# Optimization experiments

Hardware: AMD Instinct MI355X
Metric: run time of the kernel (lower is better)

## Reference

```python
import jax, jax.numpy as jnp
import numpy as np

B, S, T = 32, 128, 64
V = 32000   # src_vocab_size == tgt_vocab_size
E = 512     # rnn_input_size
H = 512     # rnn_hidden_size
PAD = 0


def lstm_cell(x, h, c, wih, whh, bih, bhh):
    # PyTorch gate order: i, f, g, o
    gates = x @ wih.T + h @ whh.T + bih + bhh
    i, f, g, o = jnp.split(gates, 4, axis=-1)
    c = jax.nn.sigmoid(f) * c + jax.nn.sigmoid(i) * jnp.tanh(g)
    h = jax.nn.sigmoid(o) * jnp.tanh(c)
    return h, c


def _encode(src, enc_emb, wih_f, whh_f, bih_f, bhh_f, wih_r, whh_r, bih_r, bhh_r):
    xs = enc_emb[src].transpose(1, 0, 2)  # [S, B, E]
    b = src.shape[0]

    def run(wih, whh, bih, bhh, reverse):
        def step(carry, x):
            h, c = carry
            h, c = lstm_cell(x, h, c, wih, whh, bih, bhh)
            return (h, c), None
        init = (jnp.zeros((b, H), xs.dtype), jnp.zeros((b, H), xs.dtype))
        (h, c), _ = jax.lax.scan(step, init, xs, reverse=reverse)
        return h, c

    hf, cf = run(wih_f, whh_f, bih_f, bhh_f, False)
    hr, cr = run(wih_r, whh_r, bih_r, bhh_r, True)
    return jnp.stack([hf, hr]), jnp.stack([cf, cr])  # (2, B, H)


def _forward(src, tgt, enc_emb, dec_emb,
             enc_wih_f, enc_whh_f, enc_bih_f, enc_bhh_f,
             enc_wih_r, enc_whh_r, enc_bih_r, enc_bhh_r,
             dec_wih_f, dec_whh_f, dec_bih_f, dec_bhh_f,
             dec_wih_r, dec_whh_r, dec_bih_r, dec_bhh_r,
             cls_w, cls_b):
    h0, c0 = _encode(src, enc_emb, enc_wih_f, enc_whh_f, enc_bih_f, enc_bhh_f,
                     enc_wih_r, enc_whh_r, enc_bih_r, enc_bhh_r)

    def step(carry, _):
        dec_in, h, c = carry
        x = dec_emb[dec_in]                      # [B, E]
        hf, cf = lstm_cell(x, h[0], c[0], dec_wih_f, dec_whh_f, dec_bih_f, dec_bhh_f)
        hr, cr = lstm_cell(x, h[1], c[1], dec_wih_r, dec_whh_r, dec_bih_r, dec_bhh_r)
        logits = jnp.concatenate([hf, hr], -1) @ cls_w.T + cls_b  # [B, V]
        nxt = jnp.argmax(logits, -1).astype(dec_in.dtype)         # sampling_ratio=0 branch
        return (nxt, jnp.stack([hf, hr]), jnp.stack([cf, cr])), logits

    init = (tgt[:, 0], h0, c0)
    _, outs = jax.lax.scan(step, init, None, length=tgt.shape[1] - 1)
    outs = outs.transpose(1, 0, 2)  # [B, T-1, V]
    zeros = jnp.zeros((tgt.shape[0], 1, outs.shape[-1]), outs.dtype)  # timestep 0 left zero
    return jnp.concatenate([zeros, outs], axis=1)  # [B, T, V]


def setup_inputs():
    key = jax.random.key(0)
    ks = jax.random.split(key, 24)
    sc = 1.0 / np.sqrt(H)

    def w(k, shape):
        return jax.random.uniform(k, shape, jnp.float32, -sc, sc)

    src = jax.random.randint(ks[0], (B, S), 0, V)
    tgt = jax.random.randint(ks[1], (B, T), 0, V)
    enc_emb = (jax.random.normal(ks[2], (V, E), jnp.float32) * 0.02).at[PAD].set(0.0)
    dec_emb = (jax.random.normal(ks[3], (V, E), jnp.float32) * 0.02).at[PAD].set(0.0)
    return {
        "src": src, "tgt": tgt,
        "enc_emb": enc_emb, "dec_emb": dec_emb,
        "enc_wih_f": w(ks[4], (4 * H, E)), "enc_whh_f": w(ks[5], (4 * H, H)),
        "enc_bih_f": w(ks[6], (4 * H,)), "enc_bhh_f": w(ks[7], (4 * H,)),
        "enc_wih_r": w(ks[8], (4 * H, E)), "enc_whh_r": w(ks[9], (4 * H, H)),
        "enc_bih_r": w(ks[10], (4 * H,)), "enc_bhh_r": w(ks[11], (4 * H,)),
        "dec_wih_f": w(ks[12], (4 * H, E)), "dec_whh_f": w(ks[13], (4 * H, H)),
        "dec_bih_f": w(ks[14], (4 * H,)), "dec_bhh_f": w(ks[15], (4 * H,)),
        "dec_wih_r": w(ks[16], (4 * H, E)), "dec_whh_r": w(ks[17], (4 * H, H)),
        "dec_bih_r": w(ks[18], (4 * H,)), "dec_bhh_r": w(ks[19], (4 * H,)),
        "cls_w": w(ks[20], (V, 2 * H)), "cls_b": w(ks[21], (V,)),
    }


def reference(src, tgt, enc_emb, dec_emb,
              enc_wih_f, enc_whh_f, enc_bih_f, enc_bhh_f,
              enc_wih_r, enc_whh_r, enc_bih_r, enc_bhh_r,
              dec_wih_f, dec_whh_f, dec_bih_f, dec_bhh_f,
              dec_wih_r, dec_whh_r, dec_bih_r, dec_bhh_r,
              cls_w, cls_b):
    return _forward(src, tgt, enc_emb, dec_emb,
                    enc_wih_f, enc_whh_f, enc_bih_f, enc_bhh_f,
                    enc_wih_r, enc_whh_r, enc_bih_r, enc_bhh_r,
                    dec_wih_f, dec_whh_f, dec_bih_f, dec_bhh_f,
                    dec_wih_r, dec_whh_r, dec_bih_r, dec_bhh_r,
                    cls_w, cls_b)
```

## Files before the change

kernel.cpp:

```cpp
#include <hip/hip_runtime.h>
#include <stdint.h>


#define NT 1024
#define NBLK 256

constexpr int HSTR = 580;
constexpr int XSTR = 1156;
constexpr unsigned LDS_ENC = 78336;
constexpr unsigned LDS_CELL = 150016;
constexpr unsigned LDS_CLS = 150528;

constexpr size_t OFF_AMAX  = 0;
constexpr size_t OFF_FLAGS = 16128;
constexpr size_t OFF_XG    = 17408;
constexpr size_t OFF_HENC  = OFF_XG + 67108864ULL;
constexpr size_t OFF_HCAT  = OFF_HENC + 262144ULL;
constexpr size_t OFF_CST   = OFF_HCAT + 262144ULL;

__device__ __forceinline__ float sigm(float x) {
  if (x >= 0.f) return 1.f / (1.f + expf(-x));
  float e = expf(x);
  return e / (1.f + e);
}

__device__ __forceinline__ void fma4(const float4& w, const float4& h, float4& a) {
  a.x = fmaf(w.x, h.x, a.x);
  a.y = fmaf(w.y, h.y, a.y);
  a.z = fmaf(w.z, h.z, a.z);
  a.w = fmaf(w.w, h.w, a.w);
}

__device__ __forceinline__ float hsum4(const float4& a) {
  return (a.x + a.y) + (a.z + a.w);
}

__device__ __forceinline__ float dot4(const float4& w, const float4& h, float acc) {
  return fmaf(w.x, h.x, fmaf(w.y, h.y, fmaf(w.z, h.z, fmaf(w.w, h.w, acc))));
}

__device__ __forceinline__ unsigned long long lgkey(float lg, int vr) {
  unsigned u = __float_as_uint(lg);
  u = (u & 0x80000000u) ? ~u : (u | 0x80000000u);
  return ((unsigned long long)u << 32) | (0xFFFFFFFFu - (unsigned)vr);
}

__global__ __launch_bounds__(NT) void k_xg(
    const int* __restrict__ src, const float* __restrict__ enc_emb,
    const float* __restrict__ ewih_f, const float* __restrict__ ebih_f,
    const float* __restrict__ ebhh_f,
    const float* __restrict__ ewih_r, const float* __restrict__ ebih_r,
    const float* __restrict__ ebhh_r,
    float* __restrict__ Xg, float* __restrict__ h_enc, float* __restrict__ out) {
  extern __shared__ float smem[];
  const int tid = threadIdx.x;
  const int bid = blockIdx.x;
  const int d  = bid >> 7;
  const int u0 = (bid & 127) << 2;

  float* hL  = smem;

  const int rgE = tid >> 7;
  const int bpE = (tid >> 4) & 7;
  const int ksE = tid & 15;
  const int r0E = rgE * 2, r1E = r0E + 1;
  const int growE0 = (r0E & 3) * 512 + u0 + (r0E >> 2);
  const int growE1 = (r1E & 3) * 512 + u0 + (r1E >> 2);

  const float* ewih = d ? ewih_r : ewih_f;
  const float* ebih = d ? ebih_r : ebih_f;
  const float* ebhh = d ? ebhh_r : ebhh_f;

  float4 wA[8], wB[8];
#pragma unroll
  for (int i4 = 0; i4 < 8; ++i4) {
    wA[i4] = *(const float4*)(ewih + (size_t)growE0 * 512 + ksE * 32 + i4 * 4);
    wB[i4] = *(const float4*)(ewih + (size_t)growE1 * 512 + ksE * 32 + i4 * 4);
  }
  const float biasA = ebih[growE0] + ebhh[growE0];
  const float biasB = ebih[growE1] + ebhh[growE1];

  for (int t = 0; t < 128; ++t) {
    {
      int b = tid >> 5, i = tid & 31;
      int tok = src[b * 128 + t];
      const float* row = enc_emb + (size_t)tok * 512;
#pragma unroll
      for (int q = 0; q < 4; ++q) {
        int k = (i + 32 * q) * 4;
        float4 v = *(const float4*)(row + k);
        int pc = k + ((k >> 5) << 2);
        *(float4*)(hL + b * HSTR + pc) = v;
      }
    }
    __syncthreads();
    for (int gi = 0; gi < 4; ++gi) {
      int b = bpE * 4 + gi;
      const float* hb = hL + b * HSTR + ksE * 36;
      float4 a0 = {0, 0, 0, 0}, a1 = {0, 0, 0, 0};
#pragma unroll
      for (int i4 = 0; i4 < 8; ++i4) {
        float4 h4 = *(const float4*)(hb + i4 * 4);
        fma4(wA[i4], h4, a0);
        fma4(wB[i4], h4, a1);
      }
      float s0 = hsum4(a0), s1 = hsum4(a1);
#pragma unroll
      for (int m = 1; m <= 8; m <<= 1) {
        s0 += __shfl_xor(s0, m, 64);
        s1 += __shfl_xor(s1, m, 64);
      }
      if (ksE == 0) {
        float* xgp = Xg + ((size_t)bid << 16) + t * 512 + b * 16;
        xgp[r0E] = s0 + biasA;
        xgp[r1E] = s1 + biasB;
      }
    }
    __syncthreads();
  }

  if (tid < 128) {
    int b = tid & 31, j = tid >> 5;
    h_enc[((0 * 2 + d) * 32 + b) * 512 + u0 + j] = 0.f;
  }
  for (int i = tid; i < 4000; i += NT) {
    int b = i & 31, vv = i >> 5;
    out[(size_t)b * 64 * 32000 + bid * 125 + vv] = 0.f;
  }
}

__global__ __launch_bounds__(NT) void k_enc(
    const float* __restrict__ ewhh_f, const float* __restrict__ ewhh_r,
    const float* __restrict__ Xg, float* __restrict__ h_enc,
    float* __restrict__ hcat, float* __restrict__ c_st, int s) {
  extern __shared__ float smem[];
  const int tid = threadIdx.x;
  const int bid = blockIdx.x;
  const int d  = bid >> 7;
  const int u0 = (bid & 127) << 2;
  const int cur = s & 1;
  const int td = d ? (127 - s) : s;

  float* hL  = smem;
  float* XgL = smem + 32 * HSTR;
  float* gL  = XgL + 512;

  const int rgE = tid >> 7;
  const int bpE = (tid >> 4) & 7;
  const int ksE = tid & 15;
  const int r0E = rgE * 2, r1E = r0E + 1;
  const int growE0 = (r0E & 3) * 512 + u0 + (r0E >> 2);
  const int growE1 = (r1E & 3) * 512 + u0 + (r1E >> 2);

  const float* ewhh = d ? ewhh_r : ewhh_f;

  float4 wA[8], wB[8];
#pragma unroll
  for (int i4 = 0; i4 < 8; ++i4) {
    wA[i4] = *(const float4*)(ewhh + (size_t)growE0 * 512 + ksE * 32 + i4 * 4);
    wB[i4] = *(const float4*)(ewhh + (size_t)growE1 * 512 + ksE * 32 + i4 * 4);
  }

  {
    int b = tid >> 5, i = tid & 31;
    const float* hr = h_enc + ((size_t)(cur * 2 + d) * 32 + b) * 512;
#pragma unroll
    for (int q = 0; q < 4; ++q) {
      int k = (i + 32 * q) * 4;
      float4 v = *(const float4*)(hr + k);
      int pc = k + ((k >> 5) << 2);
      *(float4*)(hL + b * HSTR + pc) = v;
    }
    if (tid < 128) {
      ((float4*)XgL)[tid] =
          *(const float4*)(Xg + ((size_t)bid << 16) + td * 512 + tid * 4);
    }
  }
  __syncthreads();
  for (int gi = 0; gi < 4; ++gi) {
    int b = bpE * 4 + gi;
    const float* hb = hL + b * HSTR + ksE * 36;
    float4 a0 = {0, 0, 0, 0}, a1 = {0, 0, 0, 0};
#pragma unroll
    for (int i4 = 0; i4 < 8; ++i4) {
      float4 h4 = *(const float4*)(hb + i4 * 4);
      fma4(wA[i4], h4, a0);
      fma4(wB[i4], h4, a1);
    }
    float s0 = hsum4(a0), s1 = hsum4(a1);
#pragma unroll
    for (int m = 1; m <= 8; m <<= 1) {
      s0 += __shfl_xor(s0, m, 64);
      s1 += __shfl_xor(s1, m, 64);
    }
    if (ksE == 0) {
      gL[b * 16 + r0E] = s0 + XgL[b * 16 + r0E];
      gL[b * 16 + r1E] = s1 + XgL[b * 16 + r1E];
    }
  }
  __syncthreads();
  if (tid < 128) {
    int b = tid & 31, j = tid >> 5;
    float g_i = gL[b * 16 + (j << 2) + 0];
    float g_f = gL[b * 16 + (j << 2) + 1];
    float g_g = gL[b * 16 + (j << 2) + 2];
    float g_o = gL[b * 16 + (j << 2) + 3];
    float c = (s == 0) ? 0.f : c_st[(d * 32 + b) * 512 + u0 + j];
    c = sigm(g_f) * c + sigm(g_i) * tanhf(g_g);
    float h = sigm(g_o) * tanhf(c);
    c_st[(d * 32 + b) * 512 + u0 + j] = c;
    h_enc[(((cur ^ 1) * 2 + d) * 32 + b) * 512 + u0 + j] = h;
    if (s == 127) hcat[b * 1024 + d * 512 + u0 + j] = h;
  }
}

__global__ __launch_bounds__(NT) void k_cell(
    const int* __restrict__ tgt, const float* __restrict__ dec_emb,
    const float* __restrict__ dwih_f, const float* __restrict__ dwhh_f,
    const float* __restrict__ dbih_f, const float* __restrict__ dbhh_f,
    const float* __restrict__ dwih_r, const float* __restrict__ dwhh_r,
    const float* __restrict__ dbih_r, const float* __restrict__ dbhh_r,
    float* __restrict__ hcat, float* __restrict__ c_st,
    const unsigned long long* __restrict__ amax, int t) {
  extern __shared__ float smem[];
  const int tid = threadIdx.x;
  const int bid = blockIdx.x;
  const int d  = bid >> 7;
  const int u0 = (bid & 127) << 2;
  const int p = t & 1;

  float* xhL = smem;
  float* gLd = smem + 32 * XSTR;

  const int rgD = tid >> 7;
  const int bpD = (tid >> 5) & 3;
  const int ksD = tid & 31;
  const int r0D = rgD * 2, r1D = r0D + 1;
  const int growD0 = (r0D & 3) * 512 + u0 + (r0D >> 2);
  const int growD1 = (r1D & 3) * 512 + u0 + (r1D >> 2);

  const float* dwih = d ? dwih_r : dwih_f;
  const float* dwhh = d ? dwhh_r : dwhh_f;
  const float* dbih = d ? dbih_r : dbih_f;
  const float* dbhh = d ? dbhh_r : dbhh_f;

  {
    int b = tid >> 5, i = tid & 31;
    int tok;
    if (t == 0) {
      tok = tgt[b * 64];
    } else {
      unsigned long long kv = amax[(t - 1) * 32 + b];
      tok = (int)(0xFFFFFFFFu - (unsigned)(kv & 0xFFFFFFFFull));
    }
    const float* xr = dec_emb + (size_t)tok * 512;
    const float* hr = hcat + (size_t)p * 32768 + b * 1024 + d * 512;
#pragma unroll
    for (int q = 0; q < 4; ++q) {
      int k = (i + 32 * q) * 4;
      float4 v = *(const float4*)(xr + k);
      int pc = k + ((k >> 5) << 2);
      *(float4*)(xhL + b * XSTR + pc) = v;
    }
#pragma unroll
    for (int q = 0; q < 4; ++q) {
      int k = (i + 32 * q) * 4;
      float4 v = *(const float4*)(hr + k);
      int c2 = 512 + k;
      int pc = c2 + ((c2 >> 5) << 2);
      *(float4*)(xhL + b * XSTR + pc) = v;
    }
  }
  float4 wA[8], wB[8];
  {
    const float* s0p = (ksD < 16) ? (dwih + (size_t)growD0 * 512 + ksD * 32)
                                  : (dwhh + (size_t)growD0 * 512 + (ksD - 16) * 32);
    const float* s1p = (ksD < 16) ? (dwih + (size_t)growD1 * 512 + ksD * 32)
                                  : (dwhh + (size_t)growD1 * 512 + (ksD - 16) * 32);
#pragma unroll
    for (int i4 = 0; i4 < 8; ++i4) {
      wA[i4] = *(const float4*)(s0p + i4 * 4);
      wB[i4] = *(const float4*)(s1p + i4 * 4);
    }
  }
  const float biasA = dbih[growD0] + dbhh[growD0];
  const float biasB = dbih[growD1] + dbhh[growD1];
  __syncthreads();
  for (int gi = 0; gi < 8; ++gi) {
    int b = bpD * 8 + gi;
    const float* hb = xhL + b * XSTR + ksD * 36;
    float4 a0 = {0, 0, 0, 0}, a1 = {0, 0, 0, 0};
#pragma unroll
    for (int i4 = 0; i4 < 8; ++i4) {
      float4 h4 = *(const float4*)(hb + i4 * 4);
      fma4(wA[i4], h4, a0);
      fma4(wB[i4], h4, a1);
    }
    float s0 = hsum4(a0), s1 = hsum4(a1);
#pragma unroll
    for (int m = 1; m <= 16; m <<= 1) {
      s0 += __shfl_xor(s0, m, 64);
      s1 += __shfl_xor(s1, m, 64);
    }
    if (ksD == 0) {
      gLd[b * 16 + r0D] = s0 + biasA;
      gLd[b * 16 + r1D] = s1 + biasB;
    }
  }
  __syncthreads();
  if (tid < 128) {
    int b = tid & 31, j = tid >> 5;
    float g_i = gLd[b * 16 + (j << 2) + 0];
    float g_f = gLd[b * 16 + (j << 2) + 1];
    float g_g = gLd[b * 16 + (j << 2) + 2];
    float g_o = gLd[b * 16 + (j << 2) + 3];
    float c = c_st[(d * 32 + b) * 512 + u0 + j];
    c = sigm(g_f) * c + sigm(g_i) * tanhf(g_g);
    float h = sigm(g_o) * tanhf(c);
    c_st[(d * 32 + b) * 512 + u0 + j] = c;
    hcat[(size_t)(p ^ 1) * 32768 + b * 1024 + d * 512 + u0 + j] = h;
  }
}

__global__ __launch_bounds__(NT) void k_cls(
    const float* __restrict__ cls_w, const float* __restrict__ cls_b,
    const float* __restrict__ hcat, unsigned long long* __restrict__ amax,
    float* __restrict__ out, int t) {
  extern __shared__ float smem[];
  const int tid = threadIdx.x;
  const int bid = blockIdx.x;
  const int p = t & 1;

  float* oL = smem + 32896;
  unsigned long long* amaxL = (unsigned long long*)(smem + 37504);

  {
    const float4* hr4 = (const float4*)(hcat + (size_t)(p ^ 1) * 32768);
    float4* cH4w = (float4*)smem;
#pragma unroll
    for (int q = 0; q < 8; ++q) {
      int f = tid + q * 1024;
      int b = f >> 8, k4 = f & 255;
      cH4w[b * 257 + k4] = hr4[f];
    }
    if (tid < 32) amaxL[tid] = 0ull;
  }
  __syncthreads();
  {
    const int lane = tid & 63;
    const int widu = __builtin_amdgcn_readfirstlane(tid >> 6);
    const int kc = lane & 3;
    const int bg = lane >> 2;
    const int b0 = bg * 2, b1 = b0 + 1;
    const float4* cH4 = (const float4*)smem;

    const float* wr[8];
#pragma unroll
    for (int r = 0; r < 8; ++r) {
      int lr = widu * 8 + r;
      lr = lr > 124 ? 124 : lr;
      wr[r] = cls_w + (size_t)(bid * 125 + lr) * 1024;
    }

    float acc[16];
#pragma unroll
    for (int i = 0; i < 16; ++i) acc[i] = 0.f;

    const float4* hp0 = cH4 + b0 * 257 + kc;
    const float4* hp1 = cH4 + b1 * 257 + kc;
    const int fo = kc * 4;
#pragma unroll 2
    for (int q = 0; q < 64; ++q) {
      const int ko = q * 16 + fo;
      float4 w0 = *(const float4*)(wr[0] + ko);
      float4 w1 = *(const float4*)(wr[1] + ko);
      float4 w2 = *(const float4*)(wr[2] + ko);
      float4 w3 = *(const float4*)(wr[3] + ko);
      float4 w4 = *(const float4*)(wr[4] + ko);
      float4 w5 = *(const float4*)(wr[5] + ko);
      float4 w6 = *(const float4*)(wr[6] + ko);
      float4 w7 = *(const float4*)(wr[7] + ko);
      float4 h40 = hp0[q * 4];
      float4 h41 = hp1[q * 4];
      acc[0]  = dot4(w0, h40, acc[0]);   acc[1]  = dot4(w0, h41, acc[1]);
      acc[2]  = dot4(w1, h40, acc[2]);   acc[3]  = dot4(w1, h41, acc[3]);
      acc[4]  = dot4(w2, h40, acc[4]);   acc[5]  = dot4(w2, h41, acc[5]);
      acc[6]  = dot4(w3, h40, acc[6]);   acc[7]  = dot4(w3, h41, acc[7]);
      acc[8]  = dot4(w4, h40, acc[8]);   acc[9]  = dot4(w4, h41, acc[9]);
      acc[10] = dot4(w5, h40, acc[10]);  acc[11] = dot4(w5, h41, acc[11]);
      acc[12] = dot4(w6, h40, acc[12]);  acc[13] = dot4(w6, h41, acc[13]);
      acc[14] = dot4(w7, h40, acc[14]);  acc[15] = dot4(w7, h41, acc[15]);
    }

#pragma unroll
    for (int i = 0; i < 16; ++i) {
      acc[i] += __shfl_xor(acc[i], 1, 64);
      acc[i] += __shfl_xor(acc[i], 2, 64);
    }

    float sA0, sA1, sB0, sB1;
    {
      float t0 = (kc & 1) ? acc[2]  : acc[0];
      float t1 = (kc & 1) ? acc[6]  : acc[4];
      sA0 = (kc & 2) ? t1 : t0;
      float u0v = (kc & 1) ? acc[3]  : acc[1];
      float u1v = (kc & 1) ? acc[7]  : acc[5];
      sA1 = (kc & 2) ? u1v : u0v;
      float v0v = (kc & 1) ? acc[10] : acc[8];
      float v1v = (kc & 1) ? acc[14] : acc[12];
      sB0 = (kc & 2) ? v1v : v0v;
      float w0v = (kc & 1) ? acc[11] : acc[9];
      float w1v = (kc & 1) ? acc[15] : acc[13];
      sB1 = (kc & 2) ? w1v : w0v;
    }

    const int lrA = widu * 8 + kc;
    const int lrB = lrA + 4;
    const int lrBc = lrB > 124 ? 124 : lrB;
    const int vrA = bid * 125 + lrA;
    const int vrB = bid * 125 + lrBc;
    const float cbA = cls_b[vrA];
    const float cbB = cls_b[vrB];
    const float lgA0 = sA0 + cbA, lgA1 = sA1 + cbA;
    const float lgB0 = sB0 + cbB, lgB1 = sB1 + cbB;

    oL[b0 * 130 + lrA] = lgA0;
    oL[b1 * 130 + lrA] = lgA1;
    if (lrB < 125) {
      oL[b0 * 130 + lrB] = lgB0;
      oL[b1 * 130 + lrB] = lgB1;
    }

    unsigned long long k0 = lgkey(lgA0, vrA);
    unsigned long long k1 = lgkey(lgA1, vrA);
    if (lrB < 125) {
      unsigned long long kB0 = lgkey(lgB0, vrB);
      unsigned long long kB1 = lgkey(lgB1, vrB);
      k0 = kB0 > k0 ? kB0 : k0;
      k1 = kB1 > k1 ? kB1 : k1;
    }
#pragma unroll
    for (int m = 1; m <= 2; m <<= 1) {
      unsigned long long o0 = __shfl_xor(k0, m, 64);
      unsigned long long o1 = __shfl_xor(k1, m, 64);
      k0 = o0 > k0 ? o0 : k0;
      k1 = o1 > k1 ? o1 : k1;
    }
    if (kc == 0) {
      atomicMax(&amaxL[b0], k0);
      atomicMax(&amaxL[b1], k1);
    }
  }
  __syncthreads();
#pragma unroll
  for (int it = 0; it < 4; ++it) {
    int idx = tid + it * 1024;
    int b = idx >> 7, j = idx & 127;
    if (j < 125)
      out[((size_t)b * 64 + (t + 1)) * 32000 + bid * 125 + j] = oL[b * 130 + j];
  }
  if (tid < 32) atomicMax(&amax[t * 32 + tid], amaxL[tid]);
}

extern "C" void kernel_launch(void* const* d_in, const int* in_sizes, int n_in,
                              void* d_out, int out_size, void* d_ws, size_t ws_size,
                              hipStream_t stream) {
  (void)in_sizes; (void)n_in; (void)out_size; (void)ws_size;
  const int*   src     = (const int*)d_in[0];
  const int*   tgt     = (const int*)d_in[1];
  const float* enc_emb = (const float*)d_in[2];
  const float* dec_emb = (const float*)d_in[3];
  const float* ewih_f  = (const float*)d_in[4];
  const float* ewhh_f  = (const float*)d_in[5];
  const float* ebih_f  = (const float*)d_in[6];
  const float* ebhh_f  = (const float*)d_in[7];
  const float* ewih_r  = (const float*)d_in[8];
  const float* ewhh_r  = (const float*)d_in[9];
  const float* ebih_r  = (const float*)d_in[10];
  const float* ebhh_r  = (const float*)d_in[11];
  const float* dwih_f  = (const float*)d_in[12];
  const float* dwhh_f  = (const float*)d_in[13];
  const float* dbih_f  = (const float*)d_in[14];
  const float* dbhh_f  = (const float*)d_in[15];
  const float* dwih_r  = (const float*)d_in[16];
  const float* dwhh_r  = (const float*)d_in[17];
  const float* dbih_r  = (const float*)d_in[18];
  const float* dbhh_r  = (const float*)d_in[19];
  const float* cls_w   = (const float*)d_in[20];
  const float* cls_b   = (const float*)d_in[21];

  char* ws = (char*)d_ws;
  unsigned long long* amax = (unsigned long long*)(ws + OFF_AMAX);
  float* Xg                = (float*)(ws + OFF_XG);
  float* h_enc             = (float*)(ws + OFF_HENC);
  float* hcat              = (float*)(ws + OFF_HCAT);
  float* c_st              = (float*)(ws + OFF_CST);
  float* out               = (float*)d_out;

  hipMemsetAsync(d_ws, 0, OFF_XG, stream);

  hipFuncSetAttribute((const void*)k_xg,
                      hipFuncAttributeMaxDynamicSharedMemorySize, LDS_ENC);
  hipFuncSetAttribute((const void*)k_enc,
                      hipFuncAttributeMaxDynamicSharedMemorySize, LDS_ENC);
  hipFuncSetAttribute((const void*)k_cell,
                      hipFuncAttributeMaxDynamicSharedMemorySize, LDS_CELL);
  hipFuncSetAttribute((const void*)k_cls,
                      hipFuncAttributeMaxDynamicSharedMemorySize, LDS_CLS);

  hipLaunchKernelGGL(k_xg, dim3(NBLK), dim3(NT), LDS_ENC, stream,
                     src, enc_emb, ewih_f, ebih_f, ebhh_f,
                     ewih_r, ebih_r, ebhh_r, Xg, h_enc, out);

  for (int s = 0; s < 128; ++s) {
    hipLaunchKernelGGL(k_enc, dim3(NBLK), dim3(NT), LDS_ENC, stream,
                       ewhh_f, ewhh_r, Xg, h_enc, hcat, c_st, s);
  }

  for (int t = 0; t < 63; ++t) {
    hipLaunchKernelGGL(k_cell, dim3(NBLK), dim3(NT), LDS_CELL, stream,
                       tgt, dec_emb,
                       dwih_f, dwhh_f, dbih_f, dbhh_f,
                       dwih_r, dwhh_r, dbih_r, dbhh_r,
                       hcat, c_st, amax, t);
    hipLaunchKernelGGL(k_cls, dim3(NBLK), dim3(NT), LDS_CLS, stream,
                       cls_w, cls_b, hcat, amax, out, t);
  }
}
```

Before: 7.608 ms.

## Split classifier GEMV over K halves with separate reduction kernel

```diff
diff --git a/kernel.cpp b/kernel.cpp
--- a/kernel.cpp
+++ b/kernel.cpp
@@ -9,10 +9,9 @@
 constexpr int XSTR = 1156;
 constexpr unsigned LDS_ENC = 78336;
 constexpr unsigned LDS_CELL = 150016;
-constexpr unsigned LDS_CLS = 150528;
+constexpr unsigned LDS_CLS = 66048;
 
 constexpr size_t OFF_AMAX  = 0;
-constexpr size_t OFF_FLAGS = 16128;
 constexpr size_t OFF_XG    = 17408;
 constexpr size_t OFF_HENC  = OFF_XG + 67108864ULL;
 constexpr size_t OFF_HCAT  = OFF_HENC + 262144ULL;
@@ -322,28 +321,24 @@
   }
 }
 
-__global__ __launch_bounds__(NT) void k_cls(
-    const float* __restrict__ cls_w, const float* __restrict__ cls_b,
-    const float* __restrict__ hcat, unsigned long long* __restrict__ amax,
-    float* __restrict__ out, int t) {
+__global__ __launch_bounds__(NT, 8) void k_cls(
+    const float* __restrict__ cls_w, const float* __restrict__ hcat,
+    float* __restrict__ pbuf, int t) {
   extern __shared__ float smem[];
   const int tid = threadIdx.x;
-  const int bid = blockIdx.x;
+  const int g  = blockIdx.x & 255;
+  const int kh = blockIdx.x >> 8;
   const int p = t & 1;
-
-  float* oL = smem + 32896;
-  unsigned long long* amaxL = (unsigned long long*)(smem + 37504);
 
   {
     const float4* hr4 = (const float4*)(hcat + (size_t)(p ^ 1) * 32768);
     float4* cH4w = (float4*)smem;
 #pragma unroll
-    for (int q = 0; q < 8; ++q) {
+    for (int q = 0; q < 4; ++q) {
       int f = tid + q * 1024;
-      int b = f >> 8, k4 = f & 255;
-      cH4w[b * 257 + k4] = hr4[f];
-    }
-    if (tid < 32) amaxL[tid] = 0ull;
+      int b = f >> 7, k4 = f & 127;
+      cH4w[b * 129 + k4] = hr4[b * 256 + kh * 128 + k4];
+    }
   }
   __syncthreads();
   {
@@ -359,18 +354,18 @@
     for (int r = 0; r < 8; ++r) {
       int lr = widu * 8 + r;
       lr = lr > 124 ? 124 : lr;
-      wr[r] = cls_w + (size_t)(bid * 125 + lr) * 1024;
+      wr[r] = cls_w + (size_t)(g * 125 + lr) * 1024 + kh * 512;
     }
 
     float acc[16];
 #pragma unroll
     for (int i = 0; i < 16; ++i) acc[i] = 0.f;
 
-    const float4* hp0 = cH4 + b0 * 257 + kc;
-    const float4* hp1 = cH4 + b1 * 257 + kc;
+    const float4* hp0 = cH4 + b0 * 129 + kc;
+    const float4* hp1 = cH4 + b1 * 129 + kc;
     const int fo = kc * 4;
 #pragma unroll 2
-    for (int q = 0; q < 64; ++q) {
+    for (int q = 0; q < 32; ++q) {
       const int ko = q * 16 + fo;
       float4 w0 = *(const float4*)(wr[0] + ko);
       float4 w1 = *(const float4*)(wr[1] + ko);
@@ -416,40 +411,45 @@
 
     const int lrA = widu * 8 + kc;
     const int lrB = lrA + 4;
-    const int lrBc = lrB > 124 ? 124 : lrB;
-    const int vrA = bid * 125 + lrA;
-    const int vrB = bid * 125 + lrBc;
-    const float cbA = cls_b[vrA];
-    const float cbB = cls_b[vrB];
-    const float lgA0 = sA0 + cbA, lgA1 = sA1 + cbA;
-    const float lgB0 = sB0 + cbB, lgB1 = sB1 + cbB;
-
-    oL[b0 * 130 + lrA] = lgA0;
-    oL[b1 * 130 + lrA] = lgA1;
+    float* pb = pbuf + ((size_t)(g * 2 + kh)) * 4096;
+    pb[lrA * 32 + b0] = sA0;
+    pb[lrA * 32 + b1] = sA1;
     if (lrB < 125) {
-      oL[b0 * 130 + lrB] = lgB0;
-      oL[b1 * 130 + lrB] = lgB1;
-    }
-
-    unsigned long long k0 = lgkey(lgA0, vrA);
-    unsigned long long k1 = lgkey(lgA1, vrA);
-    if (lrB < 125) {
-      unsigned long long kB0 = lgkey(lgB0, vrB);
-      unsigned long long kB1 = lgkey(lgB1, vrB);
-      k0 = kB0 > k0 ? kB0 : k0;
-      k1 = kB1 > k1 ? kB1 : k1;
-    }
-#pragma unroll
-    for (int m = 1; m <= 2; m <<= 1) {
-      unsigned long long o0 = __shfl_xor(k0, m, 64);
-      unsigned long long o1 = __shfl_xor(k1, m, 64);
-      k0 = o0 > k0 ? o0 : k0;
-      k1 = o1 > k1 ? o1 : k1;
-    }
-    if (kc == 0) {
-      atomicMax(&amaxL[b0], k0);
-      atomicMax(&amaxL[b1], k1);
-    }
+      pb[lrB * 32 + b0] = sB0;
+      pb[lrB * 32 + b1] = sB1;
+    }
+  }
+}
+
+__global__ __launch_bounds__(NT) void k_red(
+    const float* __restrict__ cls_b, const float* __restrict__ pbuf,
+    float* __restrict__ out, unsigned long long* __restrict__ amax, int t) {
+  __shared__ float trans[32 * 129];
+  __shared__ unsigned long long amaxL[32];
+  const int tid = threadIdx.x;
+  const int g = blockIdx.x;
+
+  if (tid < 32) amaxL[tid] = 0ull;
+  __syncthreads();
+  {
+    const int b = tid & 31, rq = tid >> 5;
+    const float* p0 = pbuf + (size_t)(g * 2 + 0) * 4096;
+    const float* p1 = pbuf + (size_t)(g * 2 + 1) * 4096;
+    unsigned long long bk = 0ull;
+#pragma unroll
+    for (int jj = 0; jj < 4; ++jj) {
+      int r = rq * 4 + jj;
+      if (r < 125) {
+        int vr = g * 125 + r;
+        float lg = p0[r * 32 + b] + p1[r * 32 + b] + cls_b[vr];
+        trans[b * 129 + r] = lg;
+        unsigned long long k = lgkey(lg, vr);
+        bk = k > bk ? k : bk;
+      }
+    }
+    unsigned long long o = __shfl_xor(bk, 32, 64);
+    bk = o > bk ? o : bk;
+    if ((tid & 63) < 32) atomicMax(&amaxL[b], bk);
   }
   __syncthreads();
 #pragma unroll
@@ -457,7 +457,7 @@
     int idx = tid + it * 1024;
     int b = idx >> 7, j = idx & 127;
     if (j < 125)
-      out[((size_t)b * 64 + (t + 1)) * 32000 + bid * 125 + j] = oL[b * 130 + j];
+      out[((size_t)b * 64 + (t + 1)) * 32000 + g * 125 + j] = trans[b * 129 + j];
   }
   if (tid < 32) atomicMax(&amax[t * 32 + tid], amaxL[tid]);
 }
@@ -492,6 +492,7 @@
   char* ws = (char*)d_ws;
   unsigned long long* amax = (unsigned long long*)(ws + OFF_AMAX);
   float* Xg                = (float*)(ws + OFF_XG);
+  float* pbuf              = (float*)(ws + OFF_XG);
   float* h_enc             = (float*)(ws + OFF_HENC);
   float* hcat              = (float*)(ws + OFF_HCAT);
   float* c_st              = (float*)(ws + OFF_CST);
@@ -523,7 +524,9 @@
                        dwih_f, dwhh_f, dbih_f, dbhh_f,
                        dwih_r, dwhh_r, dbih_r, dbhh_r,
                        hcat, c_st, amax, t);
-    hipLaunchKernelGGL(k_cls, dim3(NBLK), dim3(NT), LDS_CLS, stream,
-                       cls_w, cls_b, hcat, amax, out, t);
-  }
-}
+    hipLaunchKernelGGL(k_cls, dim3(NBLK * 2), dim3(NT), LDS_CLS, stream,
+                       cls_w, hcat, pbuf, t);
+    hipLaunchKernelGGL(k_red, dim3(NBLK), dim3(NT), 0, stream,
+                       cls_b, pbuf, out, amax, t);
+  }
+}
```

Result: slower. 20.30 ms (+166.8%).

## Split classifier kernel across batch halves to double block count

Applied to the files above, without the earlier changes.

```diff
diff --git a/kernel.cpp b/kernel.cpp
--- a/kernel.cpp
+++ b/kernel.cpp
@@ -9,10 +9,9 @@
 constexpr int XSTR = 1156;
 constexpr unsigned LDS_ENC = 78336;
 constexpr unsigned LDS_CELL = 150016;
-constexpr unsigned LDS_CLS = 150528;
+constexpr unsigned LDS_CLS = 74240;
 
 constexpr size_t OFF_AMAX  = 0;
-constexpr size_t OFF_FLAGS = 16128;
 constexpr size_t OFF_XG    = 17408;
 constexpr size_t OFF_HENC  = OFF_XG + 67108864ULL;
 constexpr size_t OFF_HCAT  = OFF_HENC + 262144ULL;
@@ -322,36 +321,38 @@
   }
 }
 
-__global__ __launch_bounds__(NT) void k_cls(
+__global__ __launch_bounds__(NT, 4) void k_cls(
     const float* __restrict__ cls_w, const float* __restrict__ cls_b,
     const float* __restrict__ hcat, unsigned long long* __restrict__ amax,
     float* __restrict__ out, int t) {
   extern __shared__ float smem[];
   const int tid = threadIdx.x;
-  const int bid = blockIdx.x;
+  const int n = blockIdx.x;
+  const int g  = (n >> 4) * 8 + (n & 7);
+  const int bh = (n >> 3) & 1;
   const int p = t & 1;
 
-  float* oL = smem + 32896;
-  unsigned long long* amaxL = (unsigned long long*)(smem + 37504);
+  float* oL = smem + 16448;
+  unsigned long long* amaxL = (unsigned long long*)(smem + 18528);
 
   {
     const float4* hr4 = (const float4*)(hcat + (size_t)(p ^ 1) * 32768);
     float4* cH4w = (float4*)smem;
 #pragma unroll
-    for (int q = 0; q < 8; ++q) {
+    for (int q = 0; q < 4; ++q) {
       int f = tid + q * 1024;
-      int b = f >> 8, k4 = f & 255;
-      cH4w[b * 257 + k4] = hr4[f];
-    }
-    if (tid < 32) amaxL[tid] = 0ull;
+      int lb = f >> 8, k4 = f & 255;
+      cH4w[lb * 257 + k4] = hr4[(bh * 16 + lb) * 256 + k4];
+    }
+    if (tid < 16) amaxL[tid] = 0ull;
   }
   __syncthreads();
   {
     const int lane = tid & 63;
     const int widu = __builtin_amdgcn_readfirstlane(tid >> 6);
-    const int kc = lane & 3;
-    const int bg = lane >> 2;
-    const int b0 = bg * 2, b1 = b0 + 1;
+    const int kc = lane & 7;
+    const int bg = lane >> 3;
+    const int lb0 = bg * 2, lb1 = lb0 + 1;
     const float4* cH4 = (const float4*)smem;
 
     const float* wr[8];
@@ -359,19 +360,18 @@
     for (int r = 0; r < 8; ++r) {
       int lr = widu * 8 + r;
       lr = lr > 124 ? 124 : lr;
-      wr[r] = cls_w + (size_t)(bid * 125 + lr) * 1024;
+      wr[r] = cls_w + (size_t)(g * 125 + lr) * 1024;
     }
 
     float acc[16];
 #pragma unroll
     for (int i = 0; i < 16; ++i) acc[i] = 0.f;
 
-    const float4* hp0 = cH4 + b0 * 257 + kc;
-    const float4* hp1 = cH4 + b1 * 257 + kc;
-    const int fo = kc * 4;
+    const float4* hp0 = cH4 + lb0 * 257 + kc;
+    const float4* hp1 = cH4 + lb1 * 257 + kc;
 #pragma unroll 2
-    for (int q = 0; q < 64; ++q) {
-      const int ko = q * 16 + fo;
+    for (int q = 0; q < 32; ++q) {
+      const int ko = q * 32 + kc * 4;
       float4 w0 = *(const float4*)(wr[0] + ko);
       float4 w1 = *(const float4*)(wr[1] + ko);
       float4 w2 = *(const float4*)(wr[2] + ko);
@@ -380,8 +380,8 @@
       float4 w5 = *(const float4*)(wr[5] + ko);
       float4 w6 = *(const float4*)(wr[6] + ko);
       float4 w7 = *(const float4*)(wr[7] + ko);
-      float4 h40 = hp0[q * 4];
-      float4 h41 = hp1[q * 4];
+      float4 h40 = hp0[q * 8];
+      float4 h41 = hp1[q * 8];
       acc[0]  = dot4(w0, h40, acc[0]);   acc[1]  = dot4(w0, h41, acc[1]);
       acc[2]  = dot4(w1, h40, acc[2]);   acc[3]  = dot4(w1, h41, acc[3]);
       acc[4]  = dot4(w2, h40, acc[4]);   acc[5]  = dot4(w2, h41, acc[5]);
@@ -396,70 +396,63 @@
     for (int i = 0; i < 16; ++i) {
       acc[i] += __shfl_xor(acc[i], 1, 64);
       acc[i] += __shfl_xor(acc[i], 2, 64);
-    }
-
-    float sA0, sA1, sB0, sB1;
+      acc[i] += __shfl_xor(acc[i], 4, 64);
+    }
+
+    float s0v, s1v;
     {
-      float t0 = (kc & 1) ? acc[2]  : acc[0];
-      float t1 = (kc & 1) ? acc[6]  : acc[4];
-      sA0 = (kc & 2) ? t1 : t0;
-      float u0v = (kc & 1) ? acc[3]  : acc[1];
-      float u1v = (kc & 1) ? acc[7]  : acc[5];
-      sA1 = (kc & 2) ? u1v : u0v;
-      float v0v = (kc & 1) ? acc[10] : acc[8];
-      float v1v = (kc & 1) ? acc[14] : acc[12];
-      sB0 = (kc & 2) ? v1v : v0v;
-      float w0v = (kc & 1) ? acc[11] : acc[9];
-      float w1v = (kc & 1) ? acc[15] : acc[13];
-      sB1 = (kc & 2) ? w1v : w0v;
+      float a0 = (kc & 4) ? acc[8]  : acc[0];
+      float a1 = (kc & 4) ? acc[10] : acc[2];
+      float a2 = (kc & 4) ? acc[12] : acc[4];
+      float a3 = (kc & 4) ? acc[14] : acc[6];
+      float t0 = (kc & 2) ? a2 : a0;
+      float t1 = (kc & 2) ? a3 : a1;
+      s0v = (kc & 1) ? t1 : t0;
+      float b0 = (kc & 4) ? acc[9]  : acc[1];
+      float b1 = (kc & 4) ? acc[11] : acc[3];
+      float b2 = (kc & 4) ? acc[13] : acc[5];
+      float b3 = (kc & 4) ? acc[15] : acc[7];
+      float u0 = (kc & 2) ? b2 : b0;
+      float u1 = (kc & 2) ? b3 : b1;
+      s1v = (kc & 1) ? u1 : u0;
     }
 
     const int lrA = widu * 8 + kc;
-    const int lrB = lrA + 4;
-    const int lrBc = lrB > 124 ? 124 : lrB;
-    const int vrA = bid * 125 + lrA;
-    const int vrB = bid * 125 + lrBc;
-    const float cbA = cls_b[vrA];
-    const float cbB = cls_b[vrB];
-    const float lgA0 = sA0 + cbA, lgA1 = sA1 + cbA;
-    const float lgB0 = sB0 + cbB, lgB1 = sB1 + cbB;
-
-    oL[b0 * 130 + lrA] = lgA0;
-    oL[b1 * 130 + lrA] = lgA1;
-    if (lrB < 125) {
-      oL[b0 * 130 + lrB] = lgB0;
-      oL[b1 * 130 + lrB] = lgB1;
-    }
-
-    unsigned long long k0 = lgkey(lgA0, vrA);
-    unsigned long long k1 = lgkey(lgA1, vrA);
-    if (lrB < 125) {
-      unsigned long long kB0 = lgkey(lgB0, vrB);
-      unsigned long long kB1 = lgkey(lgB1, vrB);
-      k0 = kB0 > k0 ? kB0 : k0;
-      k1 = kB1 > k1 ? kB1 : k1;
-    }
-#pragma unroll
-    for (int m = 1; m <= 2; m <<= 1) {
+    const int lrAc = lrA > 124 ? 124 : lrA;
+    const int vr = g * 125 + lrAc;
+    const float cb = cls_b[vr];
+    const float lg0 = s0v + cb;
+    const float lg1 = s1v + cb;
+
+    unsigned long long k0 = 0ull, k1 = 0ull;
+    if (lrA < 125) {
+      oL[lb0 * 130 + lrA] = lg0;
+      oL[lb1 * 130 + lrA] = lg1;
+      k0 = lgkey(lg0, vr);
+      k1 = lgkey(lg1, vr);
+    }
+#pragma unroll
+    for (int m = 1; m <= 4; m <<= 1) {
       unsigned long long o0 = __shfl_xor(k0, m, 64);
       unsigned long long o1 = __shfl_xor(k1, m, 64);
       k0 = o0 > k0 ? o0 : k0;
       k1 = o1 > k1 ? o1 : k1;
     }
     if (kc == 0) {
-      atomicMax(&amaxL[b0], k0);
-      atomicMax(&amaxL[b1], k1);
+      atomicMax(&amaxL[lb0], k0);
+      atomicMax(&amaxL[lb1], k1);
     }
   }
   __syncthreads();
 #pragma unroll
-  for (int it = 0; it < 4; ++it) {
+  for (int it = 0; it < 2; ++it) {
     int idx = tid + it * 1024;
-    int b = idx >> 7, j = idx & 127;
+    int lb = idx >> 7, j = idx & 127;
     if (j < 125)
-      out[((size_t)b * 64 + (t + 1)) * 32000 + bid * 125 + j] = oL[b * 130 + j];
-  }
-  if (tid < 32) atomicMax(&amax[t * 32 + tid], amaxL[tid]);
+      out[((size_t)(bh * 16 + lb) * 64 + (t + 1)) * 32000 + g * 125 + j] =
+          oL[lb * 130 + j];
+  }
+  if (tid < 16) atomicMax(&amax[t * 32 + bh * 16 + tid], amaxL[tid]);
 }
 
 extern "C" void kernel_launch(void* const* d_in, const int* in_sizes, int n_in,
@@ -523,7 +516,7 @@
                        dwih_f, dwhh_f, dbih_f, dbhh_f,
                        dwih_r, dwhh_r, dbih_r, dbhh_r,
                        hcat, c_st, amax, t);
-    hipLaunchKernelGGL(k_cls, dim3(NBLK), dim3(NT), LDS_CLS, stream,
+    hipLaunchKernelGGL(k_cls, dim3(NBLK * 2), dim3(NT), LDS_CLS, stream,
                        cls_w, cls_b, hcat, amax, out, t);
   }
 }
```

After: 7.731 ms. Within noise of the previous version (+1.6%).

## Restructure classifier GEMV for coalesced weight loads and add nontemporal stores

Applied to the files above, without the earlier changes.

```diff
diff --git a/kernel.cpp b/kernel.cpp
--- a/kernel.cpp
+++ b/kernel.cpp
@@ -9,14 +9,15 @@
 constexpr int XSTR = 1156;
 constexpr unsigned LDS_ENC = 78336;
 constexpr unsigned LDS_CELL = 150016;
-constexpr unsigned LDS_CLS = 150528;
+constexpr unsigned LDS_CLS = 147968;
 
 constexpr size_t OFF_AMAX  = 0;
-constexpr size_t OFF_FLAGS = 16128;
 constexpr size_t OFF_XG    = 17408;
 constexpr size_t OFF_HENC  = OFF_XG + 67108864ULL;
 constexpr size_t OFF_HCAT  = OFF_HENC + 262144ULL;
 constexpr size_t OFF_CST   = OFF_HCAT + 262144ULL;
+
+typedef float f32x4 __attribute__((ext_vector_type(4)));
 
 __device__ __forceinline__ float sigm(float x) {
   if (x >= 0.f) return 1.f / (1.f + expf(-x));
@@ -36,6 +37,10 @@
 }
 
 __device__ __forceinline__ float dot4(const float4& w, const float4& h, float acc) {
+  return fmaf(w.x, h.x, fmaf(w.y, h.y, fmaf(w.z, h.z, fmaf(w.w, h.w, acc))));
+}
+
+__device__ __forceinline__ float dot4v(const f32x4& w, const float4& h, float acc) {
   return fmaf(w.x, h.x, fmaf(w.y, h.y, fmaf(w.z, h.z, fmaf(w.w, h.w, acc))));
 }
 
@@ -125,7 +130,8 @@
   }
   for (int i = tid; i < 4000; i += NT) {
     int b = i & 31, vv = i >> 5;
-    out[(size_t)b * 64 * 32000 + bid * 125 + vv] = 0.f;
+    __builtin_nontemporal_store(0.f,
+        &out[(size_t)b * 64 * 32000 + bid * 125 + vv]);
   }
 }
 
@@ -328,11 +334,11 @@
     float* __restrict__ out, int t) {
   extern __shared__ float smem[];
   const int tid = threadIdx.x;
-  const int bid = blockIdx.x;
+  const int g = blockIdx.x;
   const int p = t & 1;
 
   float* oL = smem + 32896;
-  unsigned long long* amaxL = (unsigned long long*)(smem + 37504);
+  unsigned long long* amaxL = (unsigned long long*)(smem + 36928);
 
   {
     const float4* hr4 = (const float4*)(hcat + (size_t)(p ^ 1) * 32768);
@@ -349,106 +355,73 @@
   {
     const int lane = tid & 63;
     const int widu = __builtin_amdgcn_readfirstlane(tid >> 6);
-    const int kc = lane & 3;
-    const int bg = lane >> 2;
-    const int b0 = bg * 2, b1 = b0 + 1;
+    const int kc = lane & 15;
+    const int bg = lane >> 4;
     const float4* cH4 = (const float4*)smem;
 
-    const float* wr[8];
-#pragma unroll
-    for (int r = 0; r < 8; ++r) {
-      int lr = widu * 8 + r;
-      lr = lr > 124 ? 124 : lr;
-      wr[r] = cls_w + (size_t)(bid * 125 + lr) * 1024;
-    }
-
-    float acc[16];
-#pragma unroll
-    for (int i = 0; i < 16; ++i) acc[i] = 0.f;
-
-    const float4* hp0 = cH4 + b0 * 257 + kc;
-    const float4* hp1 = cH4 + b1 * 257 + kc;
-    const int fo = kc * 4;
+    unsigned long long bk[8];
+#pragma unroll
+    for (int j = 0; j < 8; ++j) bk[j] = 0ull;
+
+#pragma unroll
+    for (int g2 = 0; g2 < 4; ++g2) {
+      const int lrA = widu * 8 + g2 * 2;
+      const int lrB = lrA + 1;
+      const int lrAc = lrA > 124 ? 124 : lrA;
+      const int lrBc = lrB > 124 ? 124 : lrB;
+      const float* wra = cls_w + (size_t)(g * 125 + lrAc) * 1024;
+      const float* wrb = cls_w + (size_t)(g * 125 + lrBc) * 1024;
+
+      float accA[8], accB[8];
+#pragma unroll
+      for (int j = 0; j < 8; ++j) { accA[j] = 0.f; accB[j] = 0.f; }
+
 #pragma unroll 2
-    for (int q = 0; q < 64; ++q) {
-      const int ko = q * 16 + fo;
-      float4 w0 = *(const float4*)(wr[0] + ko);
-      float4 w1 = *(const float4*)(wr[1] + ko);
-      float4 w2 = *(const float4*)(wr[2] + ko);
-      float4 w3 = *(const float4*)(wr[3] + ko);
-      float4 w4 = *(const float4*)(wr[4] + ko);
-      float4 w5 = *(const float4*)(wr[5] + ko);
-      float4 w6 = *(const float4*)(wr[6] + ko);
-      float4 w7 = *(const float4*)(wr[7] + ko);
-      float4 h40 = hp0[q * 4];
-      float4 h41 = hp1[q * 4];
-      acc[0]  = dot4(w0, h40, acc[0]);   acc[1]  = dot4(w0, h41, acc[1]);
-      acc[2]  = dot4(w1, h40, acc[2]);   acc[3]  = dot4(w1, h41, acc[3]);
-      acc[4]  = dot4(w2, h40, acc[4]);   acc[5]  = dot4(w2, h41, acc[5]);
-      acc[6]  = dot4(w3, h40, acc[6]);   acc[7]  = dot4(w3, h41, acc[7]);
-      acc[8]  = dot4(w4, h40, acc[8]);   acc[9]  = dot4(w4, h41, acc[9]);
-      acc[10] = dot4(w5, h40, acc[10]);  acc[11] = dot4(w5, h41, acc[11]);
-      acc[12] = dot4(w6, h40, acc[12]);  acc[13] = dot4(w6, h41, acc[13]);
-      acc[14] = dot4(w7, h40, acc[14]);  acc[15] = dot4(w7, h41, acc[15]);
-    }
-
-#pragma unroll
-    for (int i = 0; i < 16; ++i) {
-      acc[i] += __shfl_xor(acc[i], 1, 64);
-      acc[i] += __shfl_xor(acc[i], 2, 64);
-    }
-
-    float sA0, sA1, sB0, sB1;
-    {
-      float t0 = (kc & 1) ? acc[2]  : acc[0];
-      float t1 = (kc & 1) ? acc[6]  : acc[4];
-      sA0 = (kc & 2) ? t1 : t0;
-      float u0v = (kc & 1) ? acc[3]  : acc[1];
-      float u1v = (kc & 1) ? acc[7]  : acc[5];
-      sA1 = (kc & 2) ? u1v : u0v;
-      float v0v = (kc & 1) ? acc[10] : acc[8];
-      float v1v = (kc & 1) ? acc[14] : acc[12];
-      sB0 = (kc & 2) ? v1v : v0v;
-      float w0v = (kc & 1) ? acc[11] : acc[9];
-      float w1v = (kc & 1) ? acc[15] : acc[13];
-      sB1 = (kc & 2) ? w1v : w0v;
-    }
-
-    const int lrA = widu * 8 + kc;
-    const int lrB = lrA + 4;
-    const int lrBc = lrB > 124 ? 124 : lrB;
-    const int vrA = bid * 125 + lrA;
-    const int vrB = bid * 125 + lrBc;
-    const float cbA = cls_b[vrA];
-    const float cbB = cls_b[vrB];
-    const float lgA0 = sA0 + cbA, lgA1 = sA1 + cbA;
-    const float lgB0 = sB0 + cbB, lgB1 = sB1 + cbB;
-
-    oL[b0 * 130 + lrA] = lgA0;
-    oL[b1 * 130 + lrA] = lgA1;
-    if (lrB < 125) {
-      oL[b0 * 130 + lrB] = lgB0;
-      oL[b1 * 130 + lrB] = lgB1;
-    }
-
-    unsigned long long k0 = lgkey(lgA0, vrA);
-    unsigned long long k1 = lgkey(lgA1, vrA);
-    if (lrB < 125) {
-      unsigned long long kB0 = lgkey(lgB0, vrB);
-      unsigned long long kB1 = lgkey(lgB1, vrB);
-      k0 = kB0 > k0 ? kB0 : k0;
-      k1 = kB1 > k1 ? kB1 : k1;
-    }
-#pragma unroll
-    for (int m = 1; m <= 2; m <<= 1) {
-      unsigned long long o0 = __shfl_xor(k0, m, 64);
-      unsigned long long o1 = __shfl_xor(k1, m, 64);
-      k0 = o0 > k0 ? o0 : k0;
-      k1 = o1 > k1 ? o1 : k1;
+      for (int q = 0; q < 16; ++q) {
+        const int ko = q * 64 + kc * 4;
+        f32x4 wa = __builtin_nontemporal_load((const f32x4*)(wra + ko));
+        f32x4 wb = __builtin_nontemporal_load((const f32x4*)(wrb + ko));
+#pragma unroll
+        for (int j = 0; j < 8; ++j) {
+          float4 h4 = cH4[(bg + 4 * j) * 257 + q * 16 + kc];
+          accA[j] = dot4v(wa, h4, accA[j]);
+          accB[j] = dot4v(wb, h4, accB[j]);
+        }
+      }
+
+#pragma unroll
+      for (int j = 0; j < 8; ++j) {
+#pragma unroll
+        for (int m = 1; m <= 8; m <<= 1) {
+          accA[j] += __shfl_xor(accA[j], m, 64);
+          accB[j] += __shfl_xor(accB[j], m, 64);
+        }
+      }
+
+      const int vrA = g * 125 + lrAc;
+      const int vrB = g * 125 + lrBc;
+      const float cbA = cls_b[vrA];
+      const float cbB = cls_b[vrB];
+#pragma unroll
+      for (int j = 0; j < 8; ++j) {
+        const int b = bg + 4 * j;
+        const float lgA = accA[j] + cbA;
+        const float lgB = accB[j] + cbB;
+        if (kc == 0 && lrA < 125) oL[b * 126 + lrA] = lgA;
+        if (kc == 1 && lrB < 125) oL[b * 126 + lrB] = lgB;
+        if (lrA < 125) {
+          unsigned long long kA = lgkey(lgA, vrA);
+          bk[j] = kA > bk[j] ? kA : bk[j];
+        }
+        if (lrB < 125) {
+          unsigned long long kB = lgkey(lgB, vrB);
+          bk[j] = kB > bk[j] ? kB : bk[j];
+        }
+      }
     }
     if (kc == 0) {
-      atomicMax(&amaxL[b0], k0);
-      atomicMax(&amaxL[b1], k1);
+#pragma unroll
+      for (int j = 0; j < 8; ++j) atomicMax(&amaxL[bg + 4 * j], bk[j]);
     }
   }
   __syncthreads();
@@ -457,7 +430,8 @@
     int idx = tid + it * 1024;
     int b = idx >> 7, j = idx & 127;
     if (j < 125)
-      out[((size_t)b * 64 + (t + 1)) * 32000 + bid * 125 + j] = oL[b * 130 + j];
+      __builtin_nontemporal_store(oL[b * 126 + j],
+          &out[((size_t)b * 64 + (t + 1)) * 32000 + g * 125 + j]);
   }
   if (tid < 32) atomicMax(&amax[t * 32 + tid], amaxL[tid]);
 }
```

New measurement: 7.396 ms. -2.8%, faster.
